# Performance work log

Hardware: AMD Instinct MI355X
Metric: run time of the kernel (lower is better)

## Reference

```python
import jax, jax.numpy as jnp
import numpy as np

BN_EPS = 1e-5


def setup_inputs() -> dict:
    key = jax.random.key(0)
    ks = jax.random.split(key, 4)
    N, V, C = 64, 512, 512
    K, OUT = 2, 512
    x = jax.random.normal(ks[0], (N, V, C), dtype=jnp.float32)
    A = jax.random.uniform(ks[1], (N, K, V, V), dtype=jnp.float32) / V
    conv_w = jax.random.normal(ks[2], (2 * OUT, C), dtype=jnp.float32) / np.sqrt(C)
    conv_b = jax.random.normal(ks[3], (2 * OUT,), dtype=jnp.float32) * 0.01
    gamma = jnp.ones((2 * OUT,), dtype=jnp.float32)
    beta = jnp.zeros((2 * OUT,), dtype=jnp.float32)
    eps_p = jnp.zeros((1,), dtype=jnp.float32)
    return {"x": x, "A": A, "conv_w": conv_w, "conv_b": conv_b,
            "gamma": gamma, "beta": beta, "eps_p": eps_p}


def reference(x, A, conv_w, conv_b, gamma, beta, eps_p):
    # x: (N, V, C); A: (N, K, V, V)
    N, V, C = x.shape
    K = A.shape[1]
    # 1x1 Conv1d over nodes: (N, 2*out, V)
    h = jnp.einsum('nvc,oc->nov', x, conv_w) + conv_b[None, :, None]
    # BatchNorm1d, training-mode batch stats (biased variance, per channel)
    mean = jnp.mean(h, axis=(0, 2), keepdims=True)
    var = jnp.var(h, axis=(0, 2), keepdims=True)
    h = (h - mean) * jax.lax.rsqrt(var + BN_EPS) * gamma[None, :, None] + beta[None, :, None]
    c2 = h.shape[1]
    h = h.reshape(N, K, c2 // K, V)  # (N, K, out, V)
    # graph propagation: x A then (x A) A^T, contracted over node dims
    t = jnp.einsum('nkcm,nkme->nkce', h, A)
    At = jnp.transpose(A, (0, 1, 3, 2))
    y = jnp.einsum('nkce,nkem->ncm', t, At)  # (N, out, V)
    out = (1.0 + eps_p[0]) * x + jnp.transpose(y, (0, 2, 1))
    return out, At
```

## Files before the change

kernel.cpp:

```cpp
#include <hip/hip_runtime.h>
#include <stdint.h>

typedef __bf16 bf16x8 __attribute__((ext_vector_type(8)));
typedef float f32x4 __attribute__((ext_vector_type(4)));
typedef unsigned short us8_t __attribute__((ext_vector_type(8)));

#define LDSK 40

__device__ __forceinline__ unsigned short f2bf(float f) {
  __bf16 b = (__bf16)f;
  return __builtin_bit_cast(unsigned short, b);
}
__device__ __forceinline__ float bf2f(unsigned short u) {
  union { uint32_t u; float f; } v; v.u = ((uint32_t)u) << 16;
  return v.f;
}

__device__ __forceinline__ void gload16(const void* g, void* l) {
  __builtin_amdgcn_global_load_lds(
      (const __attribute__((address_space(1))) void*)g,
      (__attribute__((address_space(3))) void*)l, 16, 0, 0);
}

__device__ __forceinline__ void stage_tile(const unsigned short* g, size_t ldg,
                                           unsigned short* lds, int wid, int lane) {
#pragma unroll
  for (int i = 0; i < 2; ++i) {
    int seg = wid * 2 + i;
    const unsigned short* gp = g + (size_t)(seg * 16 + (lane >> 2)) * ldg + (lane & 3) * 8;
    gload16(gp, lds + seg * 512);
  }
}

__device__ __forceinline__ void mfma_step(const unsigned short* As, const unsigned short* Bs,
                                          int ldb, f32x4 (*acc)[4],
                                          int wr, int wc, int lr, int lk) {
  bf16x8 a[4], b[4];
#pragma unroll
  for (int mi = 0; mi < 4; ++mi)
    a[mi] = *(const bf16x8*)(As + (wr + mi * 16 + lr) * 32 + lk * 8);
#pragma unroll
  for (int ni = 0; ni < 4; ++ni)
    b[ni] = *(const bf16x8*)(Bs + (wc + ni * 16 + lr) * ldb + lk * 8);
#pragma unroll
  for (int mi = 0; mi < 4; ++mi)
#pragma unroll
    for (int ni = 0; ni < 4; ++ni)
      acc[mi][ni] = __builtin_amdgcn_mfma_f32_16x16x32_bf16(a[mi], b[ni], acc[mi][ni], 0, 0, 0);
}

__global__ __launch_bounds__(256) void k_convert(
    const float* __restrict__ X, const float* __restrict__ W,
    unsigned short* __restrict__ Xb, unsigned short* __restrict__ Wb) {
  const size_t idx = (size_t)blockIdx.x * 256 + threadIdx.x;
  const size_t stride = (size_t)gridDim.x * 256;
  for (size_t i = idx; i < (size_t)16777216 / 8; i += stride) {
    float4 f0 = ((const float4*)X)[2 * i], f1 = ((const float4*)X)[2 * i + 1];
    us8_t w = { f2bf(f0.x), f2bf(f0.y), f2bf(f0.z), f2bf(f0.w),
                f2bf(f1.x), f2bf(f1.y), f2bf(f1.z), f2bf(f1.w) };
    ((us8_t*)Xb)[i] = w;
  }
  for (size_t i = idx; i < (size_t)524288 / 8; i += stride) {
    float4 f0 = ((const float4*)W)[2 * i], f1 = ((const float4*)W)[2 * i + 1];
    us8_t w = { f2bf(f0.x), f2bf(f0.y), f2bf(f0.z), f2bf(f0.w),
                f2bf(f1.x), f2bf(f1.y), f2bf(f1.z), f2bf(f1.w) };
    ((us8_t*)Wb)[i] = w;
  }
}

__global__ __launch_bounds__(256) void k_gemm1(
    const unsigned short* __restrict__ Wb, const unsigned short* __restrict__ Xb,
    const float* __restrict__ convb, unsigned short* __restrict__ H) {
  __shared__ unsigned short As[4096];
  __shared__ unsigned short Bs[4096];
  const int tid = threadIdx.x;
  const int L = blockIdx.x;
  const int xcd = L & 7, slot = L >> 3;
  const int n = xcd * 8 + (slot >> 5);
  const int tile = slot & 31;
  const int tm = tile >> 2, tn = tile & 3;
  const unsigned short* gA = Wb + (size_t)tm * 128 * 512;
  const unsigned short* gB = Xb + ((size_t)n * 512 + tn * 128) * 512;
  const int lane = tid & 63, wid = tid >> 6;
  const int wr = (wid >> 1) * 64, wc = (wid & 1) * 64;
  const int lr = lane & 15, lk = lane >> 4;
  f32x4 acc[4][4] = {};
  for (int k0 = 0; k0 < 512; k0 += 32) {
    stage_tile(gA + k0, 512, As, wid, lane);
    stage_tile(gB + k0, 512, Bs, wid, lane);
    __syncthreads();
    mfma_step(As, Bs, 32, acc, wr, wc, lr, lk);
    __syncthreads();
  }
  unsigned short* Hn = H + (size_t)n * 1024 * 512;
#pragma unroll
  for (int mi = 0; mi < 4; ++mi)
#pragma unroll
    for (int i = 0; i < 4; ++i) {
      int o = tm * 128 + wr + mi * 16 + lk * 4 + i;
      float bias = convb[o];
#pragma unroll
      for (int ni = 0; ni < 4; ++ni) {
        int v = tn * 128 + wc + ni * 16 + lr;
        Hn[(size_t)o * 512 + v] = f2bf(acc[mi][ni][i] + bias);
      }
    }
}

__global__ __launch_bounds__(256) void k_bn_convA(
    const unsigned short* __restrict__ H, const float* __restrict__ gamma,
    const float* __restrict__ beta, float* __restrict__ sc_sh,
    const float* __restrict__ A, unsigned short* __restrict__ Ab) {
  const int tid = threadIdx.x;
  if (blockIdx.x < 1024) {
    const int o = blockIdx.x;
    const int g = tid >> 6, l = tid & 63;
    float s1 = 0.f, s2 = 0.f;
    for (int step = 0; step < 16; ++step) {
      int n = g + step * 4;
      const us8_t* row = (const us8_t*)(H + ((size_t)n * 1024 + o) * 512);
      us8_t v = row[l];
#pragma unroll
      for (int j = 0; j < 8; ++j) { float f = bf2f(v[j]); s1 += f; s2 += f * f; }
    }
    __shared__ float r1[256], r2[256];
    r1[tid] = s1; r2[tid] = s2;
    __syncthreads();
    for (int off = 128; off > 0; off >>= 1) {
      if (tid < off) { r1[tid] += r1[tid + off]; r2[tid] += r2[tid + off]; }
      __syncthreads();
    }
    if (tid == 0) {
      float mean = r1[0] * (1.0f / 32768.0f);
      float var = r2[0] * (1.0f / 32768.0f) - mean * mean;
      float s = gamma[o] * rsqrtf(var + 1e-5f);
      sc_sh[o] = s;
      sc_sh[1024 + o] = beta[o] - mean * s;
    }
  } else {
    const size_t idx = (size_t)(blockIdx.x - 1024) * 256 + tid;
    const size_t stride = (size_t)2048 * 256;
    for (size_t i = idx; i < (size_t)33554432 / 8; i += stride) {
      float4 f0 = ((const float4*)A)[2 * i], f1 = ((const float4*)A)[2 * i + 1];
      us8_t w = { f2bf(f0.x), f2bf(f0.y), f2bf(f0.z), f2bf(f0.w),
                  f2bf(f1.x), f2bf(f1.y), f2bf(f1.z), f2bf(f1.w) };
      ((us8_t*)Ab)[i] = w;
    }
  }
}

__global__ __launch_bounds__(256) void k_bn(
    const unsigned short* __restrict__ H, const float* __restrict__ gamma,
    const float* __restrict__ beta, float* __restrict__ sc_sh) {
  const int o = blockIdx.x;
  const int tid = threadIdx.x;
  const int g = tid >> 6, l = tid & 63;
  float s1 = 0.f, s2 = 0.f;
  for (int step = 0; step < 16; ++step) {
    int n = g + step * 4;
    const us8_t* row = (const us8_t*)(H + ((size_t)n * 1024 + o) * 512);
    us8_t v = row[l];
#pragma unroll
    for (int j = 0; j < 8; ++j) { float f = bf2f(v[j]); s1 += f; s2 += f * f; }
  }
  __shared__ float r1[256], r2[256];
  r1[tid] = s1; r2[tid] = s2;
  __syncthreads();
  for (int off = 128; off > 0; off >>= 1) {
    if (tid < off) { r1[tid] += r1[tid + off]; r2[tid] += r2[tid + off]; }
    __syncthreads();
  }
  if (tid == 0) {
    float mean = r1[0] * (1.0f / 32768.0f);
    float var = r2[0] * (1.0f / 32768.0f) - mean * mean;
    float s = gamma[o] * rsqrtf(var + 1e-5f);
    sc_sh[o] = s;
    sc_sh[1024 + o] = beta[o] - mean * s;
  }
}

__global__ __launch_bounds__(256) void k_convertA(
    const float* __restrict__ A, unsigned short* __restrict__ Ab) {
  const size_t idx = (size_t)blockIdx.x * 256 + threadIdx.x;
  const size_t stride = (size_t)gridDim.x * 256;
  for (size_t i = idx; i < (size_t)33554432 / 8; i += stride) {
    float4 f0 = ((const float4*)A)[2 * i], f1 = ((const float4*)A)[2 * i + 1];
    us8_t w = { f2bf(f0.x), f2bf(f0.y), f2bf(f0.z), f2bf(f0.w),
                f2bf(f1.x), f2bf(f1.y), f2bf(f1.z), f2bf(f1.w) };
    ((us8_t*)Ab)[i] = w;
  }
}

__global__ __launch_bounds__(256) void k_affine(
    unsigned short* __restrict__ H, const float* __restrict__ sc_sh) {
  const size_t idx = (size_t)blockIdx.x * 256 + threadIdx.x;
  const size_t stride = (size_t)gridDim.x * 256;
  const size_t total8 = (size_t)64 * 1024 * 512 / 8;
  for (size_t i = idx; i < total8; i += stride) {
    size_t base = i * 8;
    int o = (int)((base >> 9) & 1023);
    float sc = sc_sh[o], sh = sc_sh[1024 + o];
    us8_t v = ((const us8_t*)H)[i];
    us8_t w;
#pragma unroll
    for (int j = 0; j < 8; ++j) w[j] = f2bf(fmaf(bf2f(v[j]), sc, sh));
    ((us8_t*)H)[i] = w;
  }
}

__global__ __launch_bounds__(256) void k_aat(
    const unsigned short* __restrict__ Ab, unsigned short* __restrict__ B2) {
  __shared__ unsigned short As[4096];
  __shared__ unsigned short Bs[4096];
  const int tid = threadIdx.x;
  const int L = blockIdx.x;
  const int xcd = L & 7, slot = L >> 3;
  const int nk = xcd * 16 + (slot >> 4);
  const int tile = slot & 15;
  const int tm = tile >> 2, tn = tile & 3;
  const unsigned short* Ank = Ab + (size_t)nk * 262144;
  const unsigned short* gA = Ank + (size_t)tm * 128 * 512;
  const unsigned short* gB = Ank + (size_t)tn * 128 * 512;
  const int lane = tid & 63, wid = tid >> 6;
  const int wr = (wid >> 1) * 64, wc = (wid & 1) * 64;
  const int lr = lane & 15, lk = lane >> 4;
  f32x4 acc[4][4] = {};
  for (int k0 = 0; k0 < 512; k0 += 32) {
    stage_tile(gA + k0, 512, As, wid, lane);
    stage_tile(gB + k0, 512, Bs, wid, lane);
    __syncthreads();
    mfma_step(As, Bs, 32, acc, wr, wc, lr, lk);
    __syncthreads();
  }
  unsigned short* Bn = B2 + (size_t)nk * 262144;
#pragma unroll
  for (int mi = 0; mi < 4; ++mi)
#pragma unroll
    for (int i = 0; i < 4; ++i) {
      int m = tm * 128 + wr + mi * 16 + lk * 4 + i;
#pragma unroll
      for (int ni = 0; ni < 4; ++ni) {
        int mp = tn * 128 + wc + ni * 16 + lr;
        Bn[(size_t)m * 512 + mp] = f2bf(acc[mi][ni][i]);
      }
    }
}

template <bool AFFINE>
__global__ __launch_bounds__(256) void k_gemm3(
    const unsigned short* __restrict__ B2, const unsigned short* __restrict__ H,
    const float* __restrict__ sc_sh, const float* __restrict__ X,
    const float* __restrict__ epsp, float* __restrict__ out) {
  __shared__ unsigned short As[4096];
  __shared__ unsigned short Bs[128 * LDSK];
  __shared__ float s_sc[2][128], s_sh[2][128];
  const int tid = threadIdx.x;
  const int L = blockIdx.x;
  const int xcd = L & 7, slot = L >> 3;
  const int n = xcd * 8 + (slot >> 4);
  const int tile = slot & 15;
  const int tm = tile >> 2, tn = tile & 3;
  const int lane = tid & 63, wid = tid >> 6;
  const int wr = (wid >> 1) * 64, wc = (wid & 1) * 64;
  const int lr = lane & 15, lk = lane >> 4;
  if (AFFINE) {
    if (tid < 256) {
      int kkq = tid >> 7, r = tid & 127;
      s_sc[kkq][r] = sc_sh[kkq * 512 + tn * 128 + r];
      s_sh[kkq][r] = sc_sh[1024 + kkq * 512 + tn * 128 + r];
    }
    __syncthreads();
  }
  f32x4 acc[4][4] = {};
  for (int kk = 0; kk < 2; ++kk) {
    const unsigned short* gA = B2 + ((size_t)(n * 2 + kk) * 512 + tm * 128) * 512;
    const unsigned short* gB = H + ((size_t)n * 1024 + kk * 512 + tn * 128) * 512;
    for (int k0 = 0; k0 < 512; k0 += 32) {
      stage_tile(gA + k0, 512, As, wid, lane);
#pragma unroll
      for (int i = 0; i < 2; ++i) {
        int s = tid + i * 256;
        int r = s >> 2, c8 = (s & 3) * 8;
        us8_t v = *(const us8_t*)(gB + (size_t)r * 512 + k0 + c8);
        if (AFFINE) {
          float sc = s_sc[kk][r], sh = s_sh[kk][r];
          us8_t w;
#pragma unroll
          for (int j = 0; j < 8; ++j) w[j] = f2bf(fmaf(bf2f(v[j]), sc, sh));
          *(us8_t*)&Bs[r * LDSK + c8] = w;
        } else {
          *(us8_t*)&Bs[r * LDSK + c8] = v;
        }
      }
      __syncthreads();
      mfma_step(As, Bs, LDSK, acc, wr, wc, lr, lk);
      __syncthreads();
    }
  }
  const float e1 = 1.0f + epsp[0];
#pragma unroll
  for (int mi = 0; mi < 4; ++mi)
#pragma unroll
    for (int i = 0; i < 4; ++i) {
      int v = tm * 128 + wr + mi * 16 + lk * 4 + i;
#pragma unroll
      for (int ni = 0; ni < 4; ++ni) {
        int c = tn * 128 + wc + ni * 16 + lr;
        size_t idx = ((size_t)n * 512 + v) * 512 + c;
        out[idx] = fmaf(e1, X[idx], acc[mi][ni][i]);
      }
    }
}

__global__ __launch_bounds__(256) void k_at(
    const float* __restrict__ A, float* __restrict__ At) {
  __shared__ float tile[64][65];
  const int nk = blockIdx.z;
  const int e0 = blockIdx.x * 64, m0 = blockIdx.y * 64;
  const float* src = A + (size_t)nk * 262144;
  float* dst = At + (size_t)nk * 262144;
  const int t = threadIdx.x;
#pragma unroll
  for (int j = 0; j < 4; ++j) {
    int ch = t + j * 256;
    int r = ch >> 4, c4 = (ch & 15) * 4;
    float4 f = *(const float4*)(src + (size_t)(m0 + r) * 512 + e0 + c4);
    tile[r][c4] = f.x; tile[r][c4 + 1] = f.y; tile[r][c4 + 2] = f.z; tile[r][c4 + 3] = f.w;
  }
  __syncthreads();
#pragma unroll
  for (int j = 0; j < 4; ++j) {
    int ch = t + j * 256;
    int e = ch >> 4, m4 = (ch & 15) * 4;
    float4 g = { tile[m4][e], tile[m4 + 1][e], tile[m4 + 2][e], tile[m4 + 3][e] };
    *(float4*)(dst + (size_t)(e0 + e) * 512 + m0 + m4) = g;
  }
}

extern "C" void kernel_launch(void* const* d_in, const int* in_sizes, int n_in,
                              void* d_out, int out_size, void* d_ws, size_t ws_size,
                              hipStream_t stream) {
  const float* x      = (const float*)d_in[0];
  const float* A      = (const float*)d_in[1];
  const float* conv_w = (const float*)d_in[2];
  const float* conv_b = (const float*)d_in[3];
  const float* gamma  = (const float*)d_in[4];
  const float* beta   = (const float*)d_in[5];
  const float* eps_p  = (const float*)d_in[6];

  float* out = (float*)d_out;
  float* At  = out + (size_t)16777216;

  unsigned short* B2 = (unsigned short*)At;
  unsigned short* H  = (unsigned short*)(At + (size_t)16777216);
  unsigned short* Xb = (unsigned short*)out;
  unsigned short* Wb = Xb + (size_t)16777216;
  unsigned short* Ab = (unsigned short*)out;

  float* wsf = (float*)d_ws;

  if (ws_size >= 8192) {
    float* sc_sh = wsf;
    k_convert    <<<2048, 256, 0, stream>>>(x, conv_w, Xb, Wb);
    k_gemm1      <<<2048, 256, 0, stream>>>(Wb, Xb, conv_b, H);
    k_bn_convA   <<<3072, 256, 0, stream>>>(H, gamma, beta, sc_sh, A, Ab);
    k_aat        <<<2048, 256, 0, stream>>>(Ab, B2);
    k_gemm3<true><<<1024, 256, 0, stream>>>(B2, H, sc_sh, x, eps_p, out);
  } else {
    float* sc_sh = out;
    k_convert     <<<2048, 256, 0, stream>>>(x, conv_w, Xb, Wb);
    k_gemm1       <<<2048, 256, 0, stream>>>(Wb, Xb, conv_b, H);
    k_bn          <<<1024, 256, 0, stream>>>(H, gamma, beta, sc_sh);
    k_affine      <<<2048, 256, 0, stream>>>(H, sc_sh);
    k_convertA    <<<2048, 256, 0, stream>>>(A, Ab);
    k_aat         <<<2048, 256, 0, stream>>>(Ab, B2);
    k_gemm3<false><<<1024, 256, 0, stream>>>(B2, H, nullptr, x, eps_p, out);
  }
  k_at<<<dim3(8, 8, 128), 256, 0, stream>>>(A, At);
}
```

Measured before the change: 296.5 us.

## Use large workspace for intermediates and fuse A transpose into BN/convert kernel

Result: faster. 276.7 us (-6.7%).

```diff
diff --git a/kernel.cpp b/kernel.cpp
--- a/kernel.cpp
+++ b/kernel.cpp
@@ -3,6 +3,7 @@
 
 typedef __bf16 bf16x8 __attribute__((ext_vector_type(8)));
 typedef float f32x4 __attribute__((ext_vector_type(4)));
+typedef unsigned short us4_t __attribute__((ext_vector_type(4)));
 typedef unsigned short us8_t __attribute__((ext_vector_type(8)));
 
 #define LDSK 40
@@ -105,6 +106,65 @@
         Hn[(size_t)o * 512 + v] = f2bf(acc[mi][ni][i] + bias);
       }
     }
+}
+
+__global__ __launch_bounds__(256) void k_bn_at_ab(
+    const unsigned short* __restrict__ H, const float* __restrict__ gamma,
+    const float* __restrict__ beta, float* __restrict__ sc_sh,
+    const float* __restrict__ A, float* __restrict__ At,
+    unsigned short* __restrict__ Ab) {
+  const int tid = threadIdx.x;
+  if (blockIdx.x < 1024) {
+    const int o = blockIdx.x;
+    const int g = tid >> 6, l = tid & 63;
+    float s1 = 0.f, s2 = 0.f;
+    for (int step = 0; step < 16; ++step) {
+      int n = g + step * 4;
+      const us8_t* row = (const us8_t*)(H + ((size_t)n * 1024 + o) * 512);
+      us8_t v = row[l];
+#pragma unroll
+      for (int j = 0; j < 8; ++j) { float f = bf2f(v[j]); s1 += f; s2 += f * f; }
+    }
+    __shared__ float r1[256], r2[256];
+    r1[tid] = s1; r2[tid] = s2;
+    __syncthreads();
+    for (int off = 128; off > 0; off >>= 1) {
+      if (tid < off) { r1[tid] += r1[tid + off]; r2[tid] += r2[tid + off]; }
+      __syncthreads();
+    }
+    if (tid == 0) {
+      float mean = r1[0] * (1.0f / 32768.0f);
+      float var = r2[0] * (1.0f / 32768.0f) - mean * mean;
+      float s = gamma[o] * rsqrtf(var + 1e-5f);
+      sc_sh[o] = s;
+      sc_sh[1024 + o] = beta[o] - mean * s;
+    }
+  } else {
+    __shared__ float tile[64][65];
+    const int tIdx = blockIdx.x - 1024;
+    const int nk = tIdx >> 6;
+    const int e0 = (tIdx & 7) * 64, m0 = ((tIdx >> 3) & 7) * 64;
+    const float* src = A + (size_t)nk * 262144;
+    float* dst = At + (size_t)nk * 262144;
+    unsigned short* ab = Ab + (size_t)nk * 262144;
+#pragma unroll
+    for (int j = 0; j < 4; ++j) {
+      int ch = tid + j * 256;
+      int r = ch >> 4, c4 = (ch & 15) * 4;
+      float4 f = *(const float4*)(src + (size_t)(m0 + r) * 512 + e0 + c4);
+      tile[r][c4] = f.x; tile[r][c4 + 1] = f.y; tile[r][c4 + 2] = f.z; tile[r][c4 + 3] = f.w;
+      us4_t u = { f2bf(f.x), f2bf(f.y), f2bf(f.z), f2bf(f.w) };
+      *(us4_t*)(ab + (size_t)(m0 + r) * 512 + e0 + c4) = u;
+    }
+    __syncthreads();
+#pragma unroll
+    for (int j = 0; j < 4; ++j) {
+      int ch = tid + j * 256;
+      int e = ch >> 4, m4 = (ch & 15) * 4;
+      float4 g = { tile[m4][e], tile[m4 + 1][e], tile[m4 + 2][e], tile[m4 + 3][e] };
+      *(float4*)(dst + (size_t)(e0 + e) * 512 + m0 + m4) = g;
+    }
+  }
 }
 
 __global__ __launch_bounds__(256) void k_bn_convA(
@@ -351,12 +411,25 @@
   float* out = (float*)d_out;
   float* At  = out + (size_t)16777216;
 
-  unsigned short* B2 = (unsigned short*)At;
-  unsigned short* H  = (unsigned short*)(At + (size_t)16777216);
   unsigned short* Xb = (unsigned short*)out;
   unsigned short* Wb = Xb + (size_t)16777216;
   unsigned short* Ab = (unsigned short*)out;
 
+  const size_t WS_BIG = (size_t)2 * 67108864 + 8192;
+  if (ws_size >= WS_BIG) {
+    unsigned short* H  = (unsigned short*)d_ws;
+    unsigned short* B2 = H + (size_t)33554432;
+    float* sc_sh = (float*)(B2 + (size_t)33554432);
+    k_convert    <<<2048, 256, 0, stream>>>(x, conv_w, Xb, Wb);
+    k_gemm1      <<<2048, 256, 0, stream>>>(Wb, Xb, conv_b, H);
+    k_bn_at_ab   <<<9216, 256, 0, stream>>>(H, gamma, beta, sc_sh, A, At, Ab);
+    k_aat        <<<2048, 256, 0, stream>>>(Ab, B2);
+    k_gemm3<true><<<1024, 256, 0, stream>>>(B2, H, sc_sh, x, eps_p, out);
+    return;
+  }
+
+  unsigned short* B2 = (unsigned short*)At;
+  unsigned short* H  = (unsigned short*)(At + (size_t)16777216);
   float* wsf = (float*)d_ws;
 
   if (ws_size >= 8192) {
```
